# Kernel optimization log

Hardware: AMD Instinct MI355X
Metric: run time of the kernel (lower is better)

The kernel has to match this reference:

```python
import jax, jax.numpy as jnp
from jax import lax
import numpy as np


def tropical_conv1d(x, w, padding, mode):
    """Tropical semiring conv1d.
    y[b,o,t] = sum_c reduce_k ( x[b,c,t+k] + w[o,c,k] )
    where reduce is min (min-plus) or max (max-plus). Zero padding like nn.Conv1d.
    x: [B, C, L], w: [O, C, K] -> y: [B, O, L + 2p - K + 1]
    """
    if padding:
        x = jnp.pad(x, ((0, 0), (0, 0), (padding, padding)))
    B, C, L = x.shape
    O, _, K = w.shape
    Lo = L - K + 1
    big = jnp.array(np.inf if mode == 'min' else -np.inf, dtype=x.dtype)
    acc0 = jnp.full((B, O, C, Lo), big, dtype=x.dtype)
    red = jnp.minimum if mode == 'min' else jnp.maximum
    wk_all = jnp.moveaxis(w, 2, 0)          # [K, O, C]
    ks = jnp.arange(K)

    def step(acc, inp):
        k, wk = inp
        xs = lax.dynamic_slice_in_dim(x, k, Lo, axis=2)      # [B, C, Lo]
        v = xs[:, None, :, :] + wk[None, :, :, None]          # [B, O, C, Lo]
        return red(acc, v), None

    acc, _ = lax.scan(step, acc0, (ks, wk_all))
    return acc.sum(axis=2)                                    # [B, O, Lo]


def avg_pool1d_2(x):
    # avg_pool1d(kernel=2, stride=2), truncating odd tail like torch
    B, C, L = x.shape
    Lh = L // 2
    return x[..., : Lh * 2].reshape(B, C, Lh, 2).mean(axis=-1)


def setup_inputs() -> dict:
    key = jax.random.key(0)
    ks = jax.random.split(key, 9)
    B, Cin, L = 64, 3, 8192
    linear_size = 32448
    s = lambda k, shape, fan: jax.random.normal(k, shape, dtype=jnp.float32) * (1.0 / np.sqrt(fan))
    return {
        'input': jax.random.normal(ks[0], (B, Cin, L), dtype=jnp.float32),
        'w1': s(ks[1], (6, Cin, 80), Cin * 80),
        'w2': s(ks[2], (16, 6, 3), 6 * 3),
        'fc1_w': s(ks[3], (120, linear_size), linear_size),
        'fc1_b': jnp.zeros((120,), jnp.float32),
        'fc2_w': s(ks[4], (84, 120), 120),
        'fc2_b': jnp.zeros((84,), jnp.float32),
        'fc3_w': s(ks[5], (10, 84), 84),
        'fc3_b': jnp.zeros((10,), jnp.float32),
    }


def reference(input, w1, w2, fc1_w, fc1_b, fc2_w, fc2_b, fc3_w, fc3_b):
    x = tropical_conv1d(input, w1, padding=2, mode='min')   # [B,6,L-75]
    x = avg_pool1d_2(x)
    x = tropical_conv1d(x, w2, padding=0, mode='max')       # [B,16,L2]
    x = avg_pool1d_2(x)
    x = x.reshape(x.shape[0], -1)                            # [B, 16*floor(L2/2)]
    x = jax.nn.relu(x @ fc1_w.T + fc1_b)
    x = jax.nn.relu(x @ fc2_w.T + fc2_b)
    return x @ fc3_w.T + fc3_b
```

## Files before the change

### kernel.cpp

```cpp
#include <hip/hip_runtime.h>

#define BB 64
#define C1 3
#define LIN 8192
#define PAD1 2
#define O1 6
#define KK1 80
#define LP1 4058

#define O2 16
#define KK2 3
#define LP2 2028

#define NFLAT 32448
#define H1 120
#define H2 84
#define NOUT 10

typedef _Float16 h2 __attribute__((ext_vector_type(2)));
typedef _Float16 f16x8 __attribute__((ext_vector_type(8)));
typedef float f32x4 __attribute__((ext_vector_type(4)));
#define BIGH ((_Float16)30000.0f)

__device__ __forceinline__ h2 bch2(float f) { return __builtin_bit_cast(h2, f); }

__global__ __launch_bounds__(256) void k_prep(const float* __restrict__ w1,
                                              float* __restrict__ whb,
                                              int* __restrict__ cnt) {
  const int idx = threadIdx.x + blockIdx.x * 256;
  if (idx == 0) *cnt = 0;
  if (idx >= (O1 * C1) * (KK1 / 2)) return;
  const int oc = idx / (KK1 / 2);
  const int m  = idx - oc * (KK1 / 2);
  h2 v;
  v.x = (_Float16)w1[oc * KK1 + 2 * m];
  v.y = (_Float16)w1[oc * KK1 + 2 * m + 1];
  whb[idx] = __builtin_bit_cast(float, v);
}

#define TILE2 127
#define NT12 16
#define DW12 295

__global__ __launch_bounds__(256) void k_conv12(const float* __restrict__ x,
                                                const float* __restrict__ whb,
                                                const float* __restrict__ w2,
                                                _Float16* __restrict__ p2h) {
  __shared__ float AB[C1][2 * DW12 + 2];
  __shared__ float ps[O1][256];
  __shared__ float w2s[O2 * O1 * KK2];
  const int tile = blockIdx.x;
  const int b    = blockIdx.y;
  const int pj0  = 2 * TILE2 * tile;
  const int T0   = 2 * pj0;
  const int tid  = threadIdx.x;

  for (int idx = tid; idx < O2 * O1 * KK2; idx += 256) w2s[idx] = w2[idx];
  for (int q = tid; q < C1 * DW12; q += 256) {
    const int c = q / DW12;
    const int d = q - c * DW12;
    const int E = T0 + 2 * d - PAD1;
    const float* xc = x + ((size_t)b * C1 + c) * LIN;
    float f0 = 0.f, f1 = 0.f, f2 = 0.f;
    if ((unsigned)E < LIN) f0 = xc[E];
    if ((unsigned)(E + 1) < LIN) f1 = xc[E + 1];
    if ((unsigned)(E + 2) < LIN) f2 = xc[E + 2];
    h2 A; A.x = (_Float16)f0; A.y = (_Float16)f1;
    h2 Bv; Bv.x = (_Float16)f1; Bv.y = (_Float16)f2;
    AB[c][2 * d]     = __builtin_bit_cast(float, A);
    AB[c][2 * d + 1] = __builtin_bit_cast(float, Bv);
  }
  __syncthreads();

  const int jj = tid;

  float s0 = 0.f, s1 = 0.f, s2 = 0.f, s3 = 0.f, s4 = 0.f, s5 = 0.f;

#pragma unroll
  for (int c = 0; c < C1; ++c) {
    h2 aA[O1], aB[O1];
#pragma unroll
    for (int o = 0; o < O1; ++o) {
      aA[o].x = BIGH; aA[o].y = BIGH;
      aB[o].x = BIGH; aB[o].y = BIGH;
    }
#pragma unroll 2
    for (int mc = 0; mc < 10; ++mc) {
      float4 xv0 = *(const float4*)&AB[c][2 * (jj + mc * 4)];
      float4 xv1 = *(const float4*)&AB[c][2 * (jj + mc * 4) + 4];
      h2 A0 = bch2(xv0.x), B0 = bch2(xv0.y);
      h2 A1 = bch2(xv0.z), B1 = bch2(xv0.w);
      h2 A2 = bch2(xv1.x), B2 = bch2(xv1.y);
      h2 A3 = bch2(xv1.z), B3 = bch2(xv1.w);
#pragma unroll
      for (int o = 0; o < O1; ++o) {
        float4 wq = *(const float4*)&whb[(o * C1 + c) * (KK1 / 2) + mc * 4];
        h2 w0 = bch2(wq.x), w1v = bch2(wq.y), w2v = bch2(wq.z), w3v = bch2(wq.w);
        aA[o] = __builtin_elementwise_min(aA[o], A0 + w0);
        aB[o] = __builtin_elementwise_min(aB[o], B0 + w0);
        aA[o] = __builtin_elementwise_min(aA[o], A1 + w1v);
        aB[o] = __builtin_elementwise_min(aB[o], B1 + w1v);
        aA[o] = __builtin_elementwise_min(aA[o], A2 + w2v);
        aB[o] = __builtin_elementwise_min(aB[o], B2 + w2v);
        aA[o] = __builtin_elementwise_min(aA[o], A3 + w3v);
        aB[o] = __builtin_elementwise_min(aB[o], B3 + w3v);
      }
    }
    float r[O1];
#pragma unroll
    for (int o = 0; o < O1; ++o)
      r[o] = fminf((float)aA[o].x, (float)aA[o].y) + fminf((float)aB[o].x, (float)aB[o].y);
    s0 += r[0]; s1 += r[1]; s2 += r[2]; s3 += r[3]; s4 += r[4]; s5 += r[5];
  }
  ps[0][jj] = 0.5f * s0;
  ps[1][jj] = 0.5f * s1;
  ps[2][jj] = 0.5f * s2;
  ps[3][jj] = 0.5f * s3;
  ps[4][jj] = 0.5f * s4;
  ps[5][jj] = 0.5f * s5;
  __syncthreads();

  const int j2i = tid & 127;
  const int ot  = tid >> 7;
  const int j2  = TILE2 * tile + j2i;
  if (j2i < TILE2 && j2 < LP2) {
    const int lb = 2 * j2i;
    float xv[O1][4];
#pragma unroll
    for (int c = 0; c < O1; ++c) {
      xv[c][0] = ps[c][lb];     xv[c][1] = ps[c][lb + 1];
      xv[c][2] = ps[c][lb + 2]; xv[c][3] = ps[c][lb + 3];
    }
#pragma unroll
    for (int oi = 0; oi < 8; ++oi) {
      const int o = ot * 8 + oi;
      float s = 0.f;
#pragma unroll
      for (int c = 0; c < O1; ++c) {
        float w0  = w2s[(o * O1 + c) * KK2 + 0];
        float w1v = w2s[(o * O1 + c) * KK2 + 1];
        float w2v = w2s[(o * O1 + c) * KK2 + 2];
        float m0 = fmaxf(fmaxf(xv[c][0] + w0, xv[c][1] + w1v), xv[c][2] + w2v);
        float m1 = fmaxf(fmaxf(xv[c][1] + w0, xv[c][2] + w1v), xv[c][3] + w2v);
        s += m0 + m1;
      }
      p2h[(size_t)b * NFLAT + o * LP2 + j2] = (_Float16)(0.5f * s);
    }
  }
}

#define KC2 128
#define NKC2 254

#define FC1_STEP(ks)                                                                     \
  {                                                                                      \
    float4 al = *(const float4*)(wp + (ks) * 32);                                        \
    float4 ah = *(const float4*)(wp + (ks) * 32 + 4);                                    \
    f16x8 A;                                                                             \
    A[0] = (_Float16)al.x; A[1] = (_Float16)al.y;                                        \
    A[2] = (_Float16)al.z; A[3] = (_Float16)al.w;                                        \
    A[4] = (_Float16)ah.x; A[5] = (_Float16)ah.y;                                        \
    A[6] = (_Float16)ah.z; A[7] = (_Float16)ah.w;                                        \
    _Pragma("unroll")                                                                    \
    for (int nt = 0; nt < 4; ++nt) {                                                     \
      f16x8 Bf = *(const f16x8*)&bs[nt * 16 + m_l][(ks) * 32 + q * 8];                   \
      acc[nt] = __builtin_amdgcn_mfma_f32_16x16x32_f16(A, Bf, acc[nt], 0, 0, 0);         \
    }                                                                                    \
  }

__global__ __launch_bounds__(512) void k_fc1(const _Float16* __restrict__ p2h,
                                             const float* __restrict__ w,
                                             _Float16* __restrict__ part) {
  __shared__ _Float16 bs[64][KC2];
  const int kc  = blockIdx.x;
  const int k0  = kc * KC2;
  const int tid = threadIdx.x;

#pragma unroll
  for (int r = 0; r < 2; ++r) {
    const int task = tid + 512 * r;
    const int row  = task >> 4;
    const int c4   = task & 15;
    const int k    = k0 + c4 * 8;
    float4 v = {0.f, 0.f, 0.f, 0.f};
    if (k + 8 <= NFLAT) v = *(const float4*)&p2h[(size_t)row * NFLAT + k];
    *(float4*)&bs[row][c4 * 8] = v;
  }
  __syncthreads();

  const int lane = tid & 63;
  const int wid  = tid >> 6;
  const int m_l  = lane & 15;
  const int q    = lane >> 4;
  const int m0   = wid * 16;

  int rowA = m0 + m_l;
  if (rowA > H1 - 1) rowA = H1 - 1;
  const float* wp = w + (size_t)rowA * NFLAT + k0 + q * 8;

  f32x4 acc[4];
#pragma unroll
  for (int nt = 0; nt < 4; ++nt) acc[nt] = (f32x4){0.f, 0.f, 0.f, 0.f};

  if (k0 + KC2 <= NFLAT) {
    FC1_STEP(0) FC1_STEP(1) FC1_STEP(2) FC1_STEP(3)
  } else {
    FC1_STEP(0) FC1_STEP(1)
  }

#pragma unroll
  for (int nt = 0; nt < 4; ++nt)
#pragma unroll
    for (int r = 0; r < 4; ++r) {
      const int i = m0 + q * 4 + r;
      if (i < H1)
        part[((size_t)kc * H1 + i) * 64 + nt * 16 + m_l] = (_Float16)acc[nt][r];
    }
}

__global__ __launch_bounds__(1024) void k_h1head(const _Float16* __restrict__ part,
                                                 const float* __restrict__ fc1_b,
                                                 const float* __restrict__ fc2_w,
                                                 const float* __restrict__ fc2_b,
                                                 const float* __restrict__ fc3_w,
                                                 const float* __restrict__ fc3_b,
                                                 float* __restrict__ h1g,
                                                 int* __restrict__ cnt,
                                                 float* __restrict__ out) {
  __shared__ float red[1024];
  __shared__ float h1s[H1 * 64];
  __shared__ float h2s[H2 * 64];
  __shared__ int   isLast;
  const int i   = blockIdx.x;
  const int tid = threadIdx.x;
  const int b   = tid & 63;
  const int sub = tid >> 6;
  float acc = 0.f;
  for (int kc = sub; kc < NKC2; kc += 16)
    acc += (float)part[((size_t)kc * H1 + i) * 64 + b];
  red[tid] = acc;
  __syncthreads();
  if (tid < 64) {
    float t = 0.f;
#pragma unroll
    for (int s2 = 0; s2 < 16; ++s2) t += red[b + 64 * s2];
    h1g[i * 64 + b] = fmaxf(t + fc1_b[i], 0.f);
  }
  __syncthreads();
  if (tid == 0) {
    __threadfence();
    isLast = (atomicAdd(cnt, 1) == H1 - 1);
  }
  __syncthreads();
  if (!isLast) return;

  __threadfence();
  for (int t = tid; t < H1 * 64; t += 1024) h1s[t] = h1g[t];
  __syncthreads();
  for (int t = tid; t < H2 * 64; t += 1024) {
    const int bb = t & 63, o = t >> 6;
    float s = fc2_b[o];
#pragma unroll 4
    for (int n = 0; n < H1; ++n) s += h1s[n * 64 + bb] * fc2_w[o * H1 + n];
    h2s[t] = fmaxf(s, 0.f);
  }
  __syncthreads();
  if (tid < NOUT * 64) {
    const int bb = tid & 63, o = tid >> 6;
    float s = fc3_b[o];
#pragma unroll 4
    for (int n = 0; n < H2; ++n) s += h2s[n * 64 + bb] * fc3_w[o * H2 + n];
    out[bb * NOUT + o] = s;
  }
}

extern "C" void kernel_launch(void* const* d_in, const int* in_sizes, int n_in,
                              void* d_out, int out_size, void* d_ws, size_t ws_size,
                              hipStream_t stream) {
  const float* x     = (const float*)d_in[0];
  const float* w1    = (const float*)d_in[1];
  const float* w2    = (const float*)d_in[2];
  const float* fc1_w = (const float*)d_in[3];
  const float* fc1_b = (const float*)d_in[4];
  const float* fc2_w = (const float*)d_in[5];
  const float* fc2_b = (const float*)d_in[6];
  const float* fc3_w = (const float*)d_in[7];
  const float* fc3_b = (const float*)d_in[8];

  _Float16* p2h  = (_Float16*)d_ws;
  _Float16* part = p2h + (size_t)BB * NFLAT;
  float*    h1g  = (float*)(part + (size_t)NKC2 * H1 * 64);
  float*    whb  = h1g + (size_t)H1 * 64;
  int*      cnt  = (int*)(whb + 720);
  float*    out  = (float*)d_out;

  hipLaunchKernelGGL(k_prep, dim3(3), dim3(256), 0, stream, w1, whb, cnt);
  hipLaunchKernelGGL(k_conv12, dim3(NT12, BB), dim3(256), 0, stream, x, whb, w2, p2h);
  hipLaunchKernelGGL(k_fc1, dim3(NKC2), dim3(512), 0, stream, p2h, fc1_w, part);
  hipLaunchKernelGGL(k_h1head, dim3(H1), dim3(1024), 0, stream, part, fc1_b, fc2_w,
                     fc2_b, fc3_w, fc3_b, h1g, cnt, out);
}
```

Baseline: 168.7 us.

## Swizzle fc1 LDS tile and split MLP head into per-batch kernel

XOR-swizzles the fc1 shared-memory B tile by row so the MFMA fragment reads spread across LDS banks instead of conflicting. It also removes the last-block atomic counter pattern: the fc2/fc3 head now runs in a separate kernel with one block per batch row, rather than in a single 1024-thread block that finishes after all h1 blocks. This adds one kernel launch but spreads the head work across many CUs and drops the serialized tail.

```diff
diff --git a/kernel.cpp b/kernel.cpp
--- a/kernel.cpp
+++ b/kernel.cpp
@@ -25,10 +25,8 @@
 __device__ __forceinline__ h2 bch2(float f) { return __builtin_bit_cast(h2, f); }
 
 __global__ __launch_bounds__(256) void k_prep(const float* __restrict__ w1,
-                                              float* __restrict__ whb,
-                                              int* __restrict__ cnt) {
+                                              float* __restrict__ whb) {
   const int idx = threadIdx.x + blockIdx.x * 256;
-  if (idx == 0) *cnt = 0;
   if (idx >= (O1 * C1) * (KK1 / 2)) return;
   const int oc = idx / (KK1 / 2);
   const int m  = idx - oc * (KK1 / 2);
@@ -151,6 +149,7 @@
 
 #define KC2 128
 #define NKC2 254
+#define BSWZ(row, colh) ((colh) ^ (((row) & 7) << 3))
 
 #define FC1_STEP(ks)                                                                     \
   {                                                                                      \
@@ -163,7 +162,8 @@
     A[6] = (_Float16)ah.z; A[7] = (_Float16)ah.w;                                        \
     _Pragma("unroll")                                                                    \
     for (int nt = 0; nt < 4; ++nt) {                                                     \
-      f16x8 Bf = *(const f16x8*)&bs[nt * 16 + m_l][(ks) * 32 + q * 8];                   \
+      const int brow = nt * 16 + m_l;                                                    \
+      f16x8 Bf = *(const f16x8*)&bs[brow][BSWZ(brow, (ks) * 32 + q * 8)];                \
       acc[nt] = __builtin_amdgcn_mfma_f32_16x16x32_f16(A, Bf, acc[nt], 0, 0, 0);         \
     }                                                                                    \
   }
@@ -184,7 +184,7 @@
     const int k    = k0 + c4 * 8;
     float4 v = {0.f, 0.f, 0.f, 0.f};
     if (k + 8 <= NFLAT) v = *(const float4*)&p2h[(size_t)row * NFLAT + k];
-    *(float4*)&bs[row][c4 * 8] = v;
+    *(float4*)&bs[row][BSWZ(row, c4 * 8)] = v;
   }
   __syncthreads();
 
@@ -218,19 +218,10 @@
     }
 }
 
-__global__ __launch_bounds__(1024) void k_h1head(const _Float16* __restrict__ part,
-                                                 const float* __restrict__ fc1_b,
-                                                 const float* __restrict__ fc2_w,
-                                                 const float* __restrict__ fc2_b,
-                                                 const float* __restrict__ fc3_w,
-                                                 const float* __restrict__ fc3_b,
-                                                 float* __restrict__ h1g,
-                                                 int* __restrict__ cnt,
-                                                 float* __restrict__ out) {
+__global__ __launch_bounds__(1024) void k_h1(const _Float16* __restrict__ part,
+                                             const float* __restrict__ fc1_b,
+                                             float* __restrict__ h1g) {
   __shared__ float red[1024];
-  __shared__ float h1s[H1 * 64];
-  __shared__ float h2s[H2 * 64];
-  __shared__ int   isLast;
   const int i   = blockIdx.x;
   const int tid = threadIdx.x;
   const int b   = tid & 63;
@@ -246,31 +237,32 @@
     for (int s2 = 0; s2 < 16; ++s2) t += red[b + 64 * s2];
     h1g[i * 64 + b] = fmaxf(t + fc1_b[i], 0.f);
   }
-  __syncthreads();
-  if (tid == 0) {
-    __threadfence();
-    isLast = (atomicAdd(cnt, 1) == H1 - 1);
-  }
-  __syncthreads();
-  if (!isLast) return;
-
-  __threadfence();
-  for (int t = tid; t < H1 * 64; t += 1024) h1s[t] = h1g[t];
-  __syncthreads();
-  for (int t = tid; t < H2 * 64; t += 1024) {
-    const int bb = t & 63, o = t >> 6;
-    float s = fc2_b[o];
+}
+
+__global__ __launch_bounds__(128) void k_head(const float* __restrict__ h1g,
+                                              const float* __restrict__ fc2_w,
+                                              const float* __restrict__ fc2_b,
+                                              const float* __restrict__ fc3_w,
+                                              const float* __restrict__ fc3_b,
+                                              float* __restrict__ out) {
+  __shared__ float h1s[H1];
+  __shared__ float h2s[H2];
+  const int b = blockIdx.x;
+  const int tid = threadIdx.x;
+  if (tid < H1) h1s[tid] = h1g[tid * 64 + b];
+  __syncthreads();
+  if (tid < H2) {
+    float s = fc2_b[tid];
 #pragma unroll 4
-    for (int n = 0; n < H1; ++n) s += h1s[n * 64 + bb] * fc2_w[o * H1 + n];
-    h2s[t] = fmaxf(s, 0.f);
-  }
-  __syncthreads();
-  if (tid < NOUT * 64) {
-    const int bb = tid & 63, o = tid >> 6;
-    float s = fc3_b[o];
+    for (int n = 0; n < H1; ++n) s += h1s[n] * fc2_w[tid * H1 + n];
+    h2s[tid] = fmaxf(s, 0.f);
+  }
+  __syncthreads();
+  if (tid < NOUT) {
+    float s = fc3_b[tid];
 #pragma unroll 4
-    for (int n = 0; n < H2; ++n) s += h2s[n * 64 + bb] * fc3_w[o * H2 + n];
-    out[bb * NOUT + o] = s;
+    for (int n = 0; n < H2; ++n) s += h2s[n] * fc3_w[tid * H2 + n];
+    out[b * NOUT + tid] = s;
   }
 }
 
@@ -291,12 +283,12 @@
   _Float16* part = p2h + (size_t)BB * NFLAT;
   float*    h1g  = (float*)(part + (size_t)NKC2 * H1 * 64);
   float*    whb  = h1g + (size_t)H1 * 64;
-  int*      cnt  = (int*)(whb + 720);
   float*    out  = (float*)d_out;
 
-  hipLaunchKernelGGL(k_prep, dim3(3), dim3(256), 0, stream, w1, whb, cnt);
+  hipLaunchKernelGGL(k_prep, dim3(3), dim3(256), 0, stream, w1, whb);
   hipLaunchKernelGGL(k_conv12, dim3(NT12, BB), dim3(256), 0, stream, x, whb, w2, p2h);
   hipLaunchKernelGGL(k_fc1, dim3(NKC2), dim3(512), 0, stream, p2h, fc1_w, part);
-  hipLaunchKernelGGL(k_h1head, dim3(H1), dim3(1024), 0, stream, part, fc1_b, fc2_w,
-                     fc2_b, fc3_w, fc3_b, h1g, cnt, out);
-}
+  hipLaunchKernelGGL(k_h1, dim3(H1), dim3(1024), 0, stream, part, fc1_b, h1g);
+  hipLaunchKernelGGL(k_head, dim3(BB), dim3(128), 0, stream, h1g, fc2_w, fc2_b,
+                     fc3_w, fc3_b, out);
+}
```

New measurement: 136.9 us. 18.8% less time.
